# Kernel optimization log

Hardware: AMD Instinct MI355X
Metric: run time of the kernel (lower is better)

## Reference

```python
import jax, jax.numpy as jnp
import numpy as np

N = 65536
DIM = 128
MARKET = 32
STYLE = 32
E = 9          # num_market_experts
TOP_K = 3
ALPHA = 1e-4


def setup_inputs() -> dict:
    key = jax.random.key(0)
    ks = jax.random.split(key, 8)
    sc = lambda k, shape, s: (jax.random.normal(k, shape, jnp.float32) * s)
    return {
        "x": jax.random.normal(ks[0], (N, 1, DIM), jnp.float32),
        # Wr: Linear(dim -> market_dim)
        "Wr_w": sc(ks[1], (DIM, MARKET), 0.05),
        "Wr_b": jnp.zeros((MARKET,), jnp.float32),
        # Wl: Linear(N -> 1), applied over the N axis
        "Wl_w": sc(ks[2], (N,), 0.005),
        "Wl_b": jnp.zeros((1,), jnp.float32),
        # router: Linear(dim + market_dim -> E)
        "router_w": sc(ks[3], (DIM + MARKET, E), 0.05),
        "router_b": jnp.zeros((E,), jnp.float32),
        # experts: style params + 2-layer MLP (dim+style -> dim -> dim)
        "styles": sc(ks[4], (E, STYLE), 1.0),
        "W1": sc(ks[5], (E, DIM + STYLE, DIM), 0.05),
        "b1": jnp.zeros((E, DIM), jnp.float32),
        "W2": sc(ks[6], (E, DIM, DIM), 0.05),
        "b2": jnp.zeros((E, DIM), jnp.float32),
    }


def reference(x, Wr_w, Wr_b, Wl_w, Wl_b, router_w, router_b, styles, W1, b1, W2, b2):
    n, s, d = x.shape  # [N, 1, dim]

    # market summary: Wr (relu MLP, dropout=identity in eval), then Wl over N axis
    market = jax.nn.relu(x @ Wr_w + Wr_b)                       # [N,1,M]
    market_g = jnp.einsum('nsm,n->sm', market, Wl_w) + Wl_b     # [1,M]
    market_exp = jnp.broadcast_to(market_g[None], (n, s, market.shape[-1]))
    x_market = jnp.concatenate([x, market_exp], axis=-1)        # [N,1,dim+M]

    # noisy-topk router (noisy=False)
    logits = x_market @ router_w + router_b                     # [N,1,E]
    _top_vals, top_idx = jax.lax.top_k(logits, TOP_K)           # [N,1,K]
    mask = (jax.nn.one_hot(top_idx, E) > 0).any(axis=-2)        # [N,1,E] bool
    sparse = jnp.where(mask, logits, -jnp.inf)
    gating = jax.nn.softmax(sparse, axis=-1)                    # [N,1,E], zeros off top-k

    # sequence-wise auxiliary load-balancing loss
    T = n * s
    flat_g = gating.reshape(-1, E)
    fi = mask.reshape(-1, E).sum(axis=0).astype(jnp.float32) * (E / (TOP_K * T))
    Pi = flat_g.mean(axis=0)
    aux_loss = ALPHA * jnp.sum(fi * Pi)

    # expert MLPs: dense-masked combine (gating is exactly 0 for unselected experts,
    # so this equals the original gather/scatter dispatch)
    flat_x = x.reshape(-1, d)                                   # [T,d]
    W1x = W1[:, :d, :]                                          # [E,d,h]
    W1s = W1[:, d:, :]                                          # [E,style,h]
    style_bias = jnp.einsum('es,esh->eh', styles, W1s) + b1     # [E,h]
    h = jax.nn.relu(jnp.einsum('nd,edh->neh', flat_x, W1x) + style_bias[None])
    out_e = jnp.einsum('neh,ehd->ned', h, W2) + b2[None]        # [T,E,d]
    out = jnp.einsum('ne,ned->nd', flat_g, out_e)               # [T,d]

    return out.reshape(n, s, d), aux_loss
```

## Files before the change

### kernel.cpp

```cpp
#include <hip/hip_runtime.h>
#include <hip/hip_bf16.h>
#include <math.h>

#define NTOK 65536
#define DIM  128
#define NE   9
#define TOPK 3
#define ALPHA_C 1e-4f

using bf16x8 = __attribute__((ext_vector_type(8))) short;
using f32x4  = __attribute__((ext_vector_type(4))) float;

static constexpr size_t OFF_MG   = 0;
static constexpr size_t OFF_CNT  = 128;
static constexpr size_t OFF_GSUM = 192;
static constexpr size_t OFF_SB   = 256;
static constexpr size_t OFF_W1F  = 4864;
static constexpr size_t OFF_W2F  = 299776;

__device__ __forceinline__ unsigned short f2bf(float f) {
    __hip_bfloat16 h = __float2bfloat16(f);
    return *reinterpret_cast<unsigned short*>(&h);
}

__global__ __launch_bounds__(256) void k_market(const float* __restrict__ x,
    const float* __restrict__ Wrw, const float* __restrict__ Wrb,
    const float* __restrict__ Wlw, float* __restrict__ mg_acc)
{
    __shared__ float xs[64 * 128];
    __shared__ float wr[128 * 32];
    __shared__ float part[256][8];
    int tid = threadIdx.x;
    int base = blockIdx.x * 64;

    const float4* x4 = (const float4*)x + (size_t)base * 32;
    float4* xs4 = (float4*)xs;
    for (int i = tid; i < 64 * 32; i += 256) xs4[i] = x4[i];
    const float4* w4 = (const float4*)Wrw;
    float4* wr4 = (float4*)wr;
    for (int i = tid; i < 128 * 32 / 4; i += 256) wr4[i] = w4[i];
    __syncthreads();

    int tok = tid >> 2, sub = tid & 3, m0 = sub * 8;
    float acc[8];
    #pragma unroll
    for (int k = 0; k < 8; ++k) acc[k] = 0.f;
    for (int d = 0; d < 128; ++d) {
        float xv = xs[tok * 128 + d];
        #pragma unroll
        for (int k = 0; k < 8; ++k) acc[k] += xv * wr[d * 32 + m0 + k];
    }
    float wl = Wlw[base + tok];
    #pragma unroll
    for (int k = 0; k < 8; ++k) {
        float v = acc[k] + Wrb[m0 + k];
        part[tid][k] = (v > 0.f ? v : 0.f) * wl;
    }
    __syncthreads();
    if (tid < 32) {
        int m = tid;
        float s = 0.f;
        for (int t = 0; t < 64; ++t) s += part[t * 4 + (m >> 3)][m & 7];
        atomicAdd(&mg_acc[m], s);
    }
}

__global__ __launch_bounds__(256) void k_prepw(const float* __restrict__ W1,
    const float* __restrict__ W2, unsigned short* __restrict__ W1F,
    unsigned short* __restrict__ W2F)
{
    int e = blockIdx.x;
    int n = blockIdx.y;
    int tid = threadIdx.x;
    int kk = tid >> 6, l = tid & 63;
    int row0 = kk * 32 + (l >> 4) * 8;
    int col  = n * 16 + (l & 15);
    const float* W1e = W1 + (size_t)e * 20480;
    const float* W2e = W2 + (size_t)e * 16384;
    size_t ob = (size_t)e * 16384 + n * 2048 + kk * 512 + l * 8;
    unsigned short u1[8], u2[8];
    #pragma unroll
    for (int j = 0; j < 8; ++j) {
        u1[j] = f2bf(W1e[(size_t)(row0 + j) * 128 + col]);
        u2[j] = f2bf(W2e[(size_t)(row0 + j) * 128 + col]);
    }
    *(ushort4*)(W1F + ob)     = *(ushort4*)(u1);
    *(ushort4*)(W1F + ob + 4) = *(ushort4*)(u1 + 4);
    *(ushort4*)(W2F + ob)     = *(ushort4*)(u2);
    *(ushort4*)(W2F + ob + 4) = *(ushort4*)(u2 + 4);
}

__global__ void k_stylebias(const float* __restrict__ styles, const float* __restrict__ W1,
                            const float* __restrict__ b1, float* __restrict__ sb)
{
    int e = blockIdx.x, h = threadIdx.x;
    float acc = b1[e * 128 + h];
    for (int s = 0; s < 32; ++s)
        acc += styles[e * 32 + s] * W1[(size_t)e * 20480 + (size_t)(128 + s) * 128 + h];
    sb[e * 128 + h] = acc;
}

__global__ void k_aux(const unsigned* __restrict__ cnt, const float* __restrict__ gsum,
                      float* __restrict__ out)
{
    float a = 0.f;
    for (int e = 0; e < 9; ++e) {
        float fi = (float)cnt[e] * ((float)NE / ((float)TOPK * (float)NTOK));
        float Pi = gsum[e] / (float)NTOK;
        a += fi * Pi;
    }
    out[(size_t)NTOK * DIM] = ALPHA_C * a;
}

__global__ __launch_bounds__(256) void k_fused(const float* __restrict__ x,
    const float* __restrict__ rweights, const float* __restrict__ rb,
    const float* __restrict__ mg, const float* __restrict__ Wlb,
    const unsigned short* __restrict__ W1F, const unsigned short* __restrict__ W2F,
    const float* __restrict__ sbg, const float* __restrict__ b2g,
    unsigned* __restrict__ cnt, float* __restrict__ gsum,
    float* __restrict__ out)
{
    __shared__ unsigned short xs[64 * 128];
    __shared__ unsigned short hs[64 * 128];
    __shared__ float garr[64][12];
    __shared__ float ce[9];
    __shared__ unsigned lcount[9];
    __shared__ float lgsum[9];

    float* part = (float*)hs;
    float* rwp  = (float*)hs + 2304;

    int tid = threadIdx.x;
    int base = blockIdx.x * 64;

    for (int i = tid; i < 160 * 9; i += 256) rwp[i] = rweights[i];
    if (tid < 9) { lcount[tid] = 0u; lgsum[tid] = 0.f; }
    __syncthreads();

    int tok = tid >> 2, sub = tid & 3;
    {
        float acc[9];
        #pragma unroll
        for (int e = 0; e < 9; ++e) acc[e] = 0.f;
        const float* xrow = x + (size_t)(base + tok) * 128 + sub * 32;
        for (int d = 0; d < 32; ++d) {
            float xv = xrow[d];
            #pragma unroll
            for (int e = 0; e < 9; ++e) acc[e] += xv * rwp[(sub * 32 + d) * 9 + e];
        }
        #pragma unroll
        for (int e = 0; e < 9; ++e) part[(tok * 4 + sub) * 9 + e] = acc[e];
    }
    if (tid < 9) {
        float c = rb[tid];
        float wlb = Wlb[0];
        for (int m = 0; m < 32; ++m) c += (mg[m] + wlb) * rwp[(128 + m) * 9 + tid];
        ce[tid] = c;
    }
    {
        const float4* x4 = (const float4*)x;
        for (int i = tid; i < 64 * 32; i += 256) {
            int row = i >> 5, p = i & 31;
            float4 v = x4[(size_t)(base + row) * 32 + p];
            unsigned short u[4] = { f2bf(v.x), f2bf(v.y), f2bf(v.z), f2bf(v.w) };
            int sw = ((((p >> 1) ^ (row & 7)) << 4) | ((p & 1) << 3));
            *(ushort4*)((char*)xs + row * 256 + sw) = *(ushort4*)u;
        }
    }
    __syncthreads();

    if (sub == 0) {
        float lg[9];
        #pragma unroll
        for (int e = 0; e < 9; ++e)
            lg[e] = ce[e] + part[(tok * 4 + 0) * 9 + e] + part[(tok * 4 + 1) * 9 + e]
                  + part[(tok * 4 + 2) * 9 + e] + part[(tok * 4 + 3) * 9 + e];
        int used = 0;
        int bi[3]; float bv[3];
        for (int k = 0; k < 3; ++k) {
            float best = -1e30f; int b = -1;
            for (int e = 0; e < 9; ++e)
                if (!((used >> e) & 1) && lg[e] > best) { best = lg[e]; b = e; }
            bi[k] = b; bv[k] = best; used |= 1 << b;
        }
        float p3[3]; float s = 0.f;
        for (int k = 0; k < 3; ++k) { p3[k] = expf(bv[k] - bv[0]); s += p3[k]; }
        #pragma unroll
        for (int e = 0; e < 12; ++e) garr[tok][e] = 0.f;
        for (int k = 0; k < 3; ++k) {
            float g = p3[k] / s;
            garr[tok][bi[k]] = g;
            atomicAdd(&lcount[bi[k]], 1u);
            atomicAdd(&lgsum[bi[k]], g);
        }
    }
    __syncthreads();
    if (tid < 9) {
        atomicAdd(&cnt[tid], lcount[tid]);
        atomicAdd(&gsum[tid], lgsum[tid]);
    }

    int lane = tid & 63, w = tid >> 6;
    int cb = lane & 15, kq = lane >> 4;

    f32x4 acc_out[4][2];
    #pragma unroll
    for (int m = 0; m < 4; ++m)
        #pragma unroll
        for (int nn = 0; nn < 2; ++nn) acc_out[m][nn] = (f32x4){0.f, 0.f, 0.f, 0.f};

    #pragma unroll 1
    for (int e = 0; e < 9; ++e) {
        const unsigned short* B1 = W1F + (size_t)e * 16384 + (w * 2) * 2048 + lane * 8;
        const unsigned short* B2 = W2F + (size_t)e * 16384 + (w * 2) * 2048 + lane * 8;

        bf16x8 b1f[2][4];
        #pragma unroll
        for (int nn = 0; nn < 2; ++nn)
            #pragma unroll
            for (int kk = 0; kk < 4; ++kk)
                b1f[nn][kk] = *(const bf16x8*)(B1 + nn * 2048 + kk * 512);

        f32x4 acc1[4][2];
        #pragma unroll
        for (int m = 0; m < 4; ++m)
            #pragma unroll
            for (int nn = 0; nn < 2; ++nn) acc1[m][nn] = (f32x4){0.f, 0.f, 0.f, 0.f};

        #pragma unroll
        for (int m = 0; m < 4; ++m) {
            int arow = m * 16 + cb;
            #pragma unroll
            for (int kk = 0; kk < 4; ++kk) {
                bf16x8 a = *(const bf16x8*)((const char*)xs + arow * 256 + ((((kk * 4 + kq) ^ (arow & 7)) << 4)));
                acc1[m][0] = __builtin_amdgcn_mfma_f32_16x16x32_bf16(a, b1f[0][kk], acc1[m][0], 0, 0, 0);
                acc1[m][1] = __builtin_amdgcn_mfma_f32_16x16x32_bf16(a, b1f[1][kk], acc1[m][1], 0, 0, 0);
            }
        }

        #pragma unroll
        for (int nn = 0; nn < 2; ++nn) {
            int col = (w * 2 + nn) * 16 + cb;
            float sbv = sbg[e * 128 + col];
            int chunk = (col * 2) >> 4;
            int boff  = (col * 2) & 15;
            #pragma unroll
            for (int m = 0; m < 4; ++m) {
                #pragma unroll
                for (int r = 0; r < 4; ++r) {
                    int row = m * 16 + kq * 4 + r;
                    float h = acc1[m][nn][r] + sbv;
                    h = (h > 0.f ? h : 0.f) * garr[row][e];
                    int sw = (((chunk ^ (row & 7)) << 4) | boff);
                    *(unsigned short*)((char*)hs + row * 256 + sw) = f2bf(h);
                }
            }
        }
        __syncthreads();

        bf16x8 b2f[2][4];
        #pragma unroll
        for (int nn = 0; nn < 2; ++nn)
            #pragma unroll
            for (int kk = 0; kk < 4; ++kk)
                b2f[nn][kk] = *(const bf16x8*)(B2 + nn * 2048 + kk * 512);

        #pragma unroll
        for (int m = 0; m < 4; ++m) {
            int arow = m * 16 + cb;
            #pragma unroll
            for (int kk = 0; kk < 4; ++kk) {
                bf16x8 a = *(const bf16x8*)((const char*)hs + arow * 256 + ((((kk * 4 + kq) ^ (arow & 7)) << 4)));
                acc_out[m][0] = __builtin_amdgcn_mfma_f32_16x16x32_bf16(a, b2f[0][kk], acc_out[m][0], 0, 0, 0);
                acc_out[m][1] = __builtin_amdgcn_mfma_f32_16x16x32_bf16(a, b2f[1][kk], acc_out[m][1], 0, 0, 0);
            }
        }
        __syncthreads();
    }

    #pragma unroll
    for (int nn = 0; nn < 2; ++nn) {
        int col = (w * 2 + nn) * 16 + cb;
        float b2c[9];
        #pragma unroll
        for (int e = 0; e < 9; ++e) b2c[e] = b2g[e * 128 + col];
        #pragma unroll
        for (int m = 0; m < 4; ++m) {
            #pragma unroll
            for (int r = 0; r < 4; ++r) {
                int row = m * 16 + kq * 4 + r;
                float bias = 0.f;
                #pragma unroll
                for (int e = 0; e < 9; ++e) bias += garr[row][e] * b2c[e];
                out[(size_t)(base + row) * 128 + col] = acc_out[m][nn][r] + bias;
            }
        }
    }
}

extern "C" void kernel_launch(void* const* d_in, const int* in_sizes, int n_in,
                              void* d_out, int out_size, void* d_ws, size_t ws_size,
                              hipStream_t stream) {
    const float* x      = (const float*)d_in[0];
    const float* Wrw    = (const float*)d_in[1];
    const float* Wrb    = (const float*)d_in[2];
    const float* Wlw    = (const float*)d_in[3];
    const float* Wlb    = (const float*)d_in[4];
    const float* rw     = (const float*)d_in[5];
    const float* rb     = (const float*)d_in[6];
    const float* styles = (const float*)d_in[7];
    const float* W1     = (const float*)d_in[8];
    const float* b1     = (const float*)d_in[9];
    const float* W2     = (const float*)d_in[10];
    const float* b2     = (const float*)d_in[11];
    float* out = (float*)d_out;

    char* ws = (char*)d_ws;
    float*          mg    = (float*)(ws + OFF_MG);
    unsigned*       cnt   = (unsigned*)(ws + OFF_CNT);
    float*          gsum  = (float*)(ws + OFF_GSUM);
    float*          sbp   = (float*)(ws + OFF_SB);
    unsigned short* W1F   = (unsigned short*)(ws + OFF_W1F);
    unsigned short* W2F   = (unsigned short*)(ws + OFF_W2F);

    hipMemsetAsync(ws, 0, 256, stream);

    k_market<<<1024, 256, 0, stream>>>(x, Wrw, Wrb, Wlw, mg);
    k_prepw<<<dim3(9, 8), 256, 0, stream>>>(W1, W2, W1F, W2F);
    k_stylebias<<<9, 128, 0, stream>>>(styles, W1, b1, sbp);
    k_fused<<<1024, 256, 0, stream>>>(x, rw, rb, mg, Wlb, W1F, W2F, sbp, b2,
                                      cnt, gsum, out);
    k_aux<<<1, 1, 0, stream>>>(cnt, gsum, out);
}
```

Before: 215.5 us.

## Swap MFMA operand roles, double-buffer hidden tile, vectorize stores, pad market LDS

```diff
diff --git a/kernel.cpp b/kernel.cpp
--- a/kernel.cpp
+++ b/kernel.cpp
@@ -27,15 +27,17 @@
     const float* __restrict__ Wrw, const float* __restrict__ Wrb,
     const float* __restrict__ Wlw, float* __restrict__ mg_acc)
 {
-    __shared__ float xs[64 * 128];
+    __shared__ float xs[64 * 132];
     __shared__ float wr[128 * 32];
     __shared__ float part[256][8];
     int tid = threadIdx.x;
     int base = blockIdx.x * 64;
 
     const float4* x4 = (const float4*)x + (size_t)base * 32;
-    float4* xs4 = (float4*)xs;
-    for (int i = tid; i < 64 * 32; i += 256) xs4[i] = x4[i];
+    for (int i = tid; i < 64 * 32; i += 256) {
+        int row = i >> 5, c4 = i & 31;
+        *(float4*)(&xs[row * 132 + c4 * 4]) = x4[i];
+    }
     const float4* w4 = (const float4*)Wrw;
     float4* wr4 = (float4*)wr;
     for (int i = tid; i < 128 * 32 / 4; i += 256) wr4[i] = w4[i];
@@ -46,7 +48,7 @@
     #pragma unroll
     for (int k = 0; k < 8; ++k) acc[k] = 0.f;
     for (int d = 0; d < 128; ++d) {
-        float xv = xs[tok * 128 + d];
+        float xv = xs[tok * 132 + d];
         #pragma unroll
         for (int k = 0; k < 8; ++k) acc[k] += xv * wr[d * 32 + m0 + k];
     }
@@ -121,7 +123,7 @@
     float* __restrict__ out)
 {
     __shared__ unsigned short xs[64 * 128];
-    __shared__ unsigned short hs[64 * 128];
+    __shared__ unsigned short hs[2][64 * 128];
     __shared__ float garr[64][12];
     __shared__ float ce[9];
     __shared__ unsigned lcount[9];
@@ -201,99 +203,107 @@
     }
 
     int lane = tid & 63, w = tid >> 6;
-    int cb = lane & 15, kq = lane >> 4;
-
-    f32x4 acc_out[4][2];
-    #pragma unroll
-    for (int m = 0; m < 4; ++m)
-        #pragma unroll
-        for (int nn = 0; nn < 2; ++nn) acc_out[m][nn] = (f32x4){0.f, 0.f, 0.f, 0.f};
+    int tl = lane & 15;
+    int hq = lane >> 4;
+    int xr = tl & 7;
+
+    f32x4 acc_out[2][4];
+    #pragma unroll
+    for (int mi = 0; mi < 2; ++mi)
+        #pragma unroll
+        for (int ni = 0; ni < 4; ++ni) acc_out[mi][ni] = (f32x4){0.f, 0.f, 0.f, 0.f};
 
     #pragma unroll 1
     for (int e = 0; e < 9; ++e) {
-        const unsigned short* B1 = W1F + (size_t)e * 16384 + (w * 2) * 2048 + lane * 8;
-        const unsigned short* B2 = W2F + (size_t)e * 16384 + (w * 2) * 2048 + lane * 8;
-
-        bf16x8 b1f[2][4];
-        #pragma unroll
-        for (int nn = 0; nn < 2; ++nn)
+        const unsigned short* A1 = W1F + (size_t)e * 16384 + (w * 2) * 2048 + lane * 8;
+        const unsigned short* A2 = W2F + (size_t)e * 16384 + (w * 2) * 2048 + lane * 8;
+        unsigned short* cur = hs[e & 1];
+
+        bf16x8 a1[2][4];
+        #pragma unroll
+        for (int mi = 0; mi < 2; ++mi)
             #pragma unroll
             for (int kk = 0; kk < 4; ++kk)
-                b1f[nn][kk] = *(const bf16x8*)(B1 + nn * 2048 + kk * 512);
-
-        f32x4 acc1[4][2];
-        #pragma unroll
-        for (int m = 0; m < 4; ++m)
-            #pragma unroll
-            for (int nn = 0; nn < 2; ++nn) acc1[m][nn] = (f32x4){0.f, 0.f, 0.f, 0.f};
-
-        #pragma unroll
-        for (int m = 0; m < 4; ++m) {
-            int arow = m * 16 + cb;
-            #pragma unroll
-            for (int kk = 0; kk < 4; ++kk) {
-                bf16x8 a = *(const bf16x8*)((const char*)xs + arow * 256 + ((((kk * 4 + kq) ^ (arow & 7)) << 4)));
-                acc1[m][0] = __builtin_amdgcn_mfma_f32_16x16x32_bf16(a, b1f[0][kk], acc1[m][0], 0, 0, 0);
-                acc1[m][1] = __builtin_amdgcn_mfma_f32_16x16x32_bf16(a, b1f[1][kk], acc1[m][1], 0, 0, 0);
+                a1[mi][kk] = *(const bf16x8*)(A1 + mi * 2048 + kk * 512);
+
+        float4 sbv0 = *(const float4*)(sbg + e * 128 + (w * 2 + 0) * 16 + hq * 4);
+        float4 sbv1 = *(const float4*)(sbg + e * 128 + (w * 2 + 1) * 16 + hq * 4);
+        f32x4 acc1[2][4];
+        #pragma unroll
+        for (int ni = 0; ni < 4; ++ni) {
+            acc1[0][ni] = (f32x4){sbv0.x, sbv0.y, sbv0.z, sbv0.w};
+            acc1[1][ni] = (f32x4){sbv1.x, sbv1.y, sbv1.z, sbv1.w};
+        }
+
+        #pragma unroll
+        for (int kk = 0; kk < 4; ++kk) {
+            #pragma unroll
+            for (int ni = 0; ni < 4; ++ni) {
+                bf16x8 b = *(const bf16x8*)((const char*)xs + (ni * 16 + tl) * 256
+                               + ((((kk * 4 + hq) ^ xr) << 4)));
+                acc1[0][ni] = __builtin_amdgcn_mfma_f32_16x16x32_bf16(a1[0][kk], b, acc1[0][ni], 0, 0, 0);
+                acc1[1][ni] = __builtin_amdgcn_mfma_f32_16x16x32_bf16(a1[1][kk], b, acc1[1][ni], 0, 0, 0);
             }
         }
 
-        #pragma unroll
-        for (int nn = 0; nn < 2; ++nn) {
-            int col = (w * 2 + nn) * 16 + cb;
-            float sbv = sbg[e * 128 + col];
-            int chunk = (col * 2) >> 4;
-            int boff  = (col * 2) & 15;
-            #pragma unroll
-            for (int m = 0; m < 4; ++m) {
-                #pragma unroll
-                for (int r = 0; r < 4; ++r) {
-                    int row = m * 16 + kq * 4 + r;
-                    float h = acc1[m][nn][r] + sbv;
-                    h = (h > 0.f ? h : 0.f) * garr[row][e];
-                    int sw = (((chunk ^ (row & 7)) << 4) | boff);
-                    *(unsigned short*)((char*)hs + row * 256 + sw) = f2bf(h);
-                }
+        bf16x8 a2[2][4];
+        #pragma unroll
+        for (int mi = 0; mi < 2; ++mi)
+            #pragma unroll
+            for (int kk = 0; kk < 4; ++kk)
+                a2[mi][kk] = *(const bf16x8*)(A2 + mi * 2048 + kk * 512);
+
+        #pragma unroll
+        for (int ni = 0; ni < 4; ++ni) {
+            int t = ni * 16 + tl;
+            float g = garr[t][e];
+            char* rowp = (char*)cur + t * 256;
+            #pragma unroll
+            for (int mi = 0; mi < 2; ++mi) {
+                f32x4 v = acc1[mi][ni];
+                unsigned short u[4];
+                u[0] = f2bf(fmaxf(v[0], 0.f) * g);
+                u[1] = f2bf(fmaxf(v[1], 0.f) * g);
+                u[2] = f2bf(fmaxf(v[2], 0.f) * g);
+                u[3] = f2bf(fmaxf(v[3], 0.f) * g);
+                int chunk = (w * 2 + mi) * 2 + (hq >> 1);
+                int off = (hq & 1) * 8;
+                *(ushort4*)(rowp + (((chunk ^ xr) << 4) | off)) = *(ushort4*)u;
             }
         }
         __syncthreads();
 
-        bf16x8 b2f[2][4];
-        #pragma unroll
-        for (int nn = 0; nn < 2; ++nn)
-            #pragma unroll
-            for (int kk = 0; kk < 4; ++kk)
-                b2f[nn][kk] = *(const bf16x8*)(B2 + nn * 2048 + kk * 512);
-
-        #pragma unroll
-        for (int m = 0; m < 4; ++m) {
-            int arow = m * 16 + cb;
-            #pragma unroll
-            for (int kk = 0; kk < 4; ++kk) {
-                bf16x8 a = *(const bf16x8*)((const char*)hs + arow * 256 + ((((kk * 4 + kq) ^ (arow & 7)) << 4)));
-                acc_out[m][0] = __builtin_amdgcn_mfma_f32_16x16x32_bf16(a, b2f[0][kk], acc_out[m][0], 0, 0, 0);
-                acc_out[m][1] = __builtin_amdgcn_mfma_f32_16x16x32_bf16(a, b2f[1][kk], acc_out[m][1], 0, 0, 0);
+        #pragma unroll
+        for (int kk = 0; kk < 4; ++kk) {
+            #pragma unroll
+            for (int ni = 0; ni < 4; ++ni) {
+                bf16x8 b = *(const bf16x8*)((const char*)cur + (ni * 16 + tl) * 256
+                               + ((((kk * 4 + hq) ^ xr) << 4)));
+                acc_out[0][ni] = __builtin_amdgcn_mfma_f32_16x16x32_bf16(a2[0][kk], b, acc_out[0][ni], 0, 0, 0);
+                acc_out[1][ni] = __builtin_amdgcn_mfma_f32_16x16x32_bf16(a2[1][kk], b, acc_out[1][ni], 0, 0, 0);
             }
         }
-        __syncthreads();
-    }
-
-    #pragma unroll
-    for (int nn = 0; nn < 2; ++nn) {
-        int col = (w * 2 + nn) * 16 + cb;
-        float b2c[9];
-        #pragma unroll
-        for (int e = 0; e < 9; ++e) b2c[e] = b2g[e * 128 + col];
-        #pragma unroll
-        for (int m = 0; m < 4; ++m) {
-            #pragma unroll
-            for (int r = 0; r < 4; ++r) {
-                int row = m * 16 + kq * 4 + r;
-                float bias = 0.f;
-                #pragma unroll
-                for (int e = 0; e < 9; ++e) bias += garr[row][e] * b2c[e];
-                out[(size_t)(base + row) * 128 + col] = acc_out[m][nn][r] + bias;
+    }
+
+    #pragma unroll
+    for (int mi = 0; mi < 2; ++mi) {
+        int d0 = (w * 2 + mi) * 16 + hq * 4;
+        float4 b2v[9];
+        #pragma unroll
+        for (int e = 0; e < 9; ++e) b2v[e] = *(const float4*)(b2g + e * 128 + d0);
+        #pragma unroll
+        for (int ni = 0; ni < 4; ++ni) {
+            int t = ni * 16 + tl;
+            float4 bias = {0.f, 0.f, 0.f, 0.f};
+            #pragma unroll
+            for (int e = 0; e < 9; ++e) {
+                float g = garr[t][e];
+                bias.x += g * b2v[e].x; bias.y += g * b2v[e].y;
+                bias.z += g * b2v[e].z; bias.w += g * b2v[e].w;
             }
+            f32x4 v = acc_out[mi][ni];
+            float4 r = {v[0] + bias.x, v[1] + bias.y, v[2] + bias.z, v[3] + bias.w};
+            *(float4*)(out + (size_t)(base + t) * 128 + d0) = r;
         }
     }
 }
```

Result: faster. 199.3 us (-7.5%).
